# Performance work log

Measured on AMD Instinct MI355X. Metric: run time of the kernel, lower is better.

The kernel has to match this reference:

```python
import jax, jax.numpy as jnp
import numpy as np

EPS = 1e-5


def _bn_relu(h, gamma, beta):
    # BatchNorm1d in training mode: stats over all but the last (channel) dim
    m = h.reshape(-1, h.shape[-1])
    mu = jnp.mean(m, axis=0)
    var = jnp.var(m, axis=0)
    return jax.nn.relu((h - mu) * jax.lax.rsqrt(var + EPS) * gamma + beta)


def setup_inputs() -> dict:
    key = jax.random.key(0)
    ks = jax.random.split(key, 16)
    B, N, D, OUT = 64, 64, 64, 128
    T = 2 * D          # object_tuple_size = 128
    HG, HF = 256, 128  # hidden_dim_g, hidden_dim_f

    def lin(k, i, o):
        return (jax.random.normal(k, (i, o), jnp.float32) / np.sqrt(i).astype(np.float32),
                jnp.zeros((o,), jnp.float32))

    inp = {"x": jax.random.normal(ks[0], (B, N, D), jnp.float32)}
    # G: depth-3 Linear-BN-ReLU, dims T -> HG -> HG -> T
    for i, (a, b) in enumerate([(T, HG), (HG, HG), (HG, T)]):
        W, bb = lin(ks[1 + i], a, b)
        inp[f"gW{i}"] = W
        inp[f"gb{i}"] = bb
        inp[f"gg{i}"] = jnp.ones((b,), jnp.float32)
        inp[f"gB{i}"] = jnp.zeros((b,), jnp.float32)
    # F: depth-2 Linear-BN-ReLU, dims T -> HF -> T, then Linear(T, OUT)
    for i, (a, b) in enumerate([(T, HF), (HF, T)]):
        W, bb = lin(ks[5 + i], a, b)
        inp[f"fW{i}"] = W
        inp[f"fb{i}"] = bb
        inp[f"fg{i}"] = jnp.ones((b,), jnp.float32)
        inp[f"fB{i}"] = jnp.zeros((b,), jnp.float32)
    inp["foW"], inp["fob"] = lin(ks[8], T, OUT)
    return inp


def reference(x, gW0, gb0, gg0, gB0, gW1, gb1, gg1, gB1, gW2, gb2, gg2, gB2,
              fW0, fb0, fg0, fB0, fW1, fb1, fg1, fB1, foW, fob):
    B, N, D = x.shape
    # GroupObjectsIntoPairs: all ordered pairs -> (B, N*N, 2D)
    xi = jnp.broadcast_to(x[:, :, None, :], (B, N, N, D))
    xj = jnp.broadcast_to(x[:, None, :, :], (B, N, N, D))
    h = jnp.concatenate([xi, xj], axis=-1).reshape(B, N * N, 2 * D)
    # G: per-pair MLP
    for W, b, g, be in ((gW0, gb0, gg0, gB0), (gW1, gb1, gg1, gB1), (gW2, gb2, gg2, gB2)):
        h = _bn_relu(h @ W + b, g, be)
    # sum over pair dimension (no layer norm)
    s = h.sum(axis=1)  # (B, 2D)
    # F: MLP + final linear
    for W, b, g, be in ((fW0, fb0, fg0, fB0), (fW1, fb1, fg1, fB1)):
        s = _bn_relu(s @ W + b, g, be)
    return s @ foW + fob  # (B, OUT)
```

## Files before the change

kernel.cpp:

```cpp
#include <hip/hip_runtime.h>


typedef _Float16 half8 __attribute__((ext_vector_type(8)));
typedef _Float16 half4_t __attribute__((ext_vector_type(4)));
typedef float float4_t __attribute__((ext_vector_type(4)));
typedef float float2_t __attribute__((ext_vector_type(2)));
typedef unsigned int uint2_t __attribute__((ext_vector_type(2)));

static constexpr float kEps = 1e-5f;
static constexpr float kM = 262144.f;

static constexpr size_t OFF_U   = 0;
static constexpr size_t OFF_V   = OFF_U  + (size_t)4096*256*4;
static constexpr size_t OFF_UP  = OFF_V  + (size_t)4096*256*4;
static constexpr size_t OFF_VP  = OFF_UP + (size_t)4096*256*2;
static constexpr size_t OFF_W1T = OFF_VP + (size_t)4096*256*2;
static constexpr size_t OFF_W2T = OFF_W1T + (size_t)256*256*2;
static constexpr size_t OFF_Z1  = OFF_W2T + (size_t)128*256*2;
static constexpr size_t OFF_C0S = OFF_Z1 + (size_t)262144*256;
static constexpr size_t OFF_C0T = OFF_C0S + 1024;
static constexpr size_t OFF_ST0 = OFF_C0T + 1024;
static constexpr size_t OFF_ST1 = OFF_ST0 + (size_t)64*4*256*4;
static constexpr size_t OFF_ST2 = OFF_ST1 + (size_t)32*512*4;
static constexpr size_t OFF_SB  = OFF_ST2 + (size_t)32*256*4;
static constexpr size_t OFF_FST0 = OFF_SB + (size_t)64*128*4;
static constexpr size_t OFF_FST1 = OFF_FST0 + 1024;
static constexpr int ZERO_FLOATS = (64*4*256 + 32*512 + 32*256 + 64*128 + 256 + 256);
static constexpr size_t OFF_FZ0  = OFF_FST1 + 1024;
static constexpr size_t OFF_FZ1  = OFF_FZ0 + (size_t)64*128*4;
static constexpr size_t OFF_Z2   = OFF_FZ1 + (size_t)64*128*4;

static __device__ inline half8 relu8(half8 s) {
#pragma unroll
  for (int e = 0; e < 8; ++e) s[e] = s[e] > (_Float16)0 ? s[e] : (_Float16)0;
  return s;
}

static __device__ inline uint2_t pack_fp8x8(half8 hv) {
  int lo = 0, hi = 0;
  lo = __builtin_amdgcn_cvt_pk_fp8_f32((float)hv[0], (float)hv[1], lo, false);
  lo = __builtin_amdgcn_cvt_pk_fp8_f32((float)hv[2], (float)hv[3], lo, true);
  hi = __builtin_amdgcn_cvt_pk_fp8_f32((float)hv[4], (float)hv[5], hi, false);
  hi = __builtin_amdgcn_cvt_pk_fp8_f32((float)hv[6], (float)hv[7], hi, true);
  uint2_t o = {(unsigned)lo, (unsigned)hi};
  return o;
}

__global__ __launch_bounds__(256) void k_wt(const float* __restrict__ gW1,
                                            const float* __restrict__ gW2,
                                            _Float16* __restrict__ W1T,
                                            _Float16* __restrict__ W2T,
                                            float* __restrict__ zbuf) {
  int idx = blockIdx.x * 256 + threadIdx.x;
  if (idx < 65536) {
    int n = idx >> 8, k = idx & 255;
    W1T[idx] = (_Float16)gW1[k * 256 + n];
  } else if (idx < 98304) {
    int j = idx - 65536;
    int n = j >> 8, k = j & 255;
    W2T[j] = (_Float16)gW2[k * 128 + n];
  }
  if (idx < ZERO_FLOATS) zbuf[idx] = 0.f;
}

__global__ __launch_bounds__(256) void k_prep(const float* __restrict__ x,
                                              const float* __restrict__ gW0,
                                              float* __restrict__ U,
                                              float* __restrict__ V,
                                              float* __restrict__ st0) {
  __shared__ __align__(16) float sX[32 * 64];
  __shared__ __align__(16) float sZ[32 * 128];
  int t = threadIdx.x;
  int p0 = blockIdx.x * 32;
  int by = blockIdx.y;
  int hsel = by >> 1;
  int cbase = (by & 1) * 128;
#pragma unroll
  for (int it = 0; it < 2; ++it) {
    int f4 = (it * 256 + t) * 4;
    *(float4_t*)(sX + f4) = *(const float4_t*)(x + (size_t)p0 * 64 + f4);
  }
  __syncthreads();
  int r = t >> 3, cg = (t & 7) * 16;
  const float* Wb = gW0 + (size_t)(hsel * 64) * 256 + cbase + cg;
  float acc[16];
#pragma unroll
  for (int j = 0; j < 16; ++j) acc[j] = 0.f;
  for (int k = 0; k < 64; ++k) {
    float xv = sX[r * 64 + k];
    const float4_t* wr = (const float4_t*)(Wb + (size_t)k * 256);
    float4_t w0 = wr[0], w1 = wr[1], w2 = wr[2], w3 = wr[3];
#pragma unroll
    for (int j = 0; j < 4; ++j) {
      acc[j]      += xv * w0[j];
      acc[4 + j]  += xv * w1[j];
      acc[8 + j]  += xv * w2[j];
      acc[12 + j] += xv * w3[j];
    }
  }
  float* outp = (hsel ? V : U) + (size_t)(p0 + r) * 256 + cbase + cg;
#pragma unroll
  for (int q = 0; q < 4; ++q) {
    float4_t o = {acc[q * 4], acc[q * 4 + 1], acc[q * 4 + 2], acc[q * 4 + 3]};
    *(float4_t*)(outp + q * 4) = o;
  }
#pragma unroll
  for (int j = 0; j < 16; ++j) sZ[r * 128 + cg + j] = acc[j];
  __syncthreads();
  if (t < 128) {
    float S = 0.f, S2 = 0.f;
#pragma unroll
    for (int rr = 0; rr < 32; ++rr) {
      float z = sZ[rr * 128 + t];
      S += z;
      S2 += z * z;
    }
    int b = blockIdx.x >> 1;
    atomicAdd(st0 + (size_t)(b * 4 + hsel * 2 + 0) * 256 + cbase + t, S);
    atomicAdd(st0 + (size_t)(b * 4 + hsel * 2 + 1) * 256 + cbase + t, S2);
  }
}

__global__ __launch_bounds__(256) void k_bn0(const float* __restrict__ st0,
                                             const float* __restrict__ gb0,
                                             const float* __restrict__ gg0,
                                             const float* __restrict__ gB0,
                                             float* __restrict__ c0s,
                                             float* __restrict__ c0t) {
  int c = threadIdx.x;
  float su = 0, su2 = 0, sv = 0, sv2 = 0, cross = 0;
  for (int b = 0; b < 64; ++b) {
    float a  = st0[(b * 4 + 0) * 256 + c];
    float a2 = st0[(b * 4 + 1) * 256 + c];
    float v  = st0[(b * 4 + 2) * 256 + c];
    float v2 = st0[(b * 4 + 3) * 256 + c];
    su += a; su2 += a2; sv += v; sv2 += v2; cross += a * v;
  }
  float b0 = gb0[c];
  float sumz  = 64.f * (su + sv) + kM * b0;
  float sumzz = 64.f * (su2 + sv2) + 2.f * cross + 2.f * b0 * 64.f * (su + sv) + kM * b0 * b0;
  float mu = sumz / kM;
  float var = sumzz / kM - mu * mu;
  float sc = gg0[c] * rsqrtf(var + kEps);
  c0s[c] = sc;
  c0t[c] = gB0[c] + sc * (b0 - mu);
}

__global__ __launch_bounds__(256) void k_uv(const float* __restrict__ U,
                                            const float* __restrict__ V,
                                            const float* __restrict__ c0s,
                                            const float* __restrict__ c0t,
                                            _Float16* __restrict__ Up,
                                            _Float16* __restrict__ Vp) {
  int idx = blockIdx.x * 256 + threadIdx.x;
  int e4 = idx * 4;
  int c4 = e4 & 255;
  float4_t u = *(const float4_t*)(U + e4);
  float4_t v = *(const float4_t*)(V + e4);
  float4_t s = *(const float4_t*)(c0s + c4);
  float4_t tt = *(const float4_t*)(c0t + c4);
  half4_t hu, hv;
#pragma unroll
  for (int e = 0; e < 4; ++e) {
    hu[e] = (_Float16)(u[e] * s[e] + tt[e]);
    hv[e] = (_Float16)(v[e] * s[e]);
  }
  *(half4_t*)(Up + e4) = hu;
  *(half4_t*)(Vp + e4) = hv;
}

__global__ __launch_bounds__(256) void k_gemm1(const _Float16* __restrict__ Up,
                                               const _Float16* __restrict__ Vp,
                                               const _Float16* __restrict__ W1T,
                                               const float* __restrict__ gb1,
                                               unsigned char* __restrict__ Z1,
                                               float* __restrict__ stats1) {
  __shared__ __align__(16) char smem[2 * 128 * 72 * 2];
  _Float16* sA = (_Float16*)smem;
  _Float16* sW = (_Float16*)(smem + 128 * 72 * 2);
  _Float16* sO = (_Float16*)smem;

  const int t = threadIdx.x;
  const int bx = blockIdx.x;
  const int n0 = blockIdx.y * 128;
  const int b = bx >> 5;
  const int i0 = (bx & 31) * 2;
  const long R0 = (long)bx * 128;

  const int wid = t >> 6, L = t & 63;
  const int wrow = wid >> 1, wcol = wid & 1;
  const int quad = L >> 4, l15 = L & 15;

  const int prow = t >> 2;
  const int pk = (t & 3) * 16;

  const _Float16* UpI0 = Up + (size_t)(b * 64 + i0) * 256;
  const _Float16* UpI1 = UpI0 + 256;
  const _Float16* VpJ  = Vp + (size_t)(b * 64 + prow) * 256;

  float4_t acc[4][4];
#pragma unroll
  for (int mt = 0; mt < 4; ++mt)
#pragma unroll
    for (int nt = 0; nt < 4; ++nt) acc[mt][nt] = (float4_t){0.f, 0.f, 0.f, 0.f};

  for (int kc = 0; kc < 4; ++kc) {
    __syncthreads();
    {
      const int kg = kc * 64 + pk;
      half8 va = *(const half8*)(VpJ + kg);
      half8 vb = *(const half8*)(VpJ + kg + 8);
      half8 u0a = *(const half8*)(UpI0 + kg);
      half8 u0b = *(const half8*)(UpI0 + kg + 8);
      half8 u1a = *(const half8*)(UpI1 + kg);
      half8 u1b = *(const half8*)(UpI1 + kg + 8);
      *(half8*)(sA + prow * 72 + pk)            = relu8(u0a + va);
      *(half8*)(sA + prow * 72 + pk + 8)        = relu8(u0b + vb);
      *(half8*)(sA + (64 + prow) * 72 + pk)     = relu8(u1a + va);
      *(half8*)(sA + (64 + prow) * 72 + pk + 8) = relu8(u1b + vb);
    }
#pragma unroll
    for (int it = 0; it < 4; ++it) {
      int flat = it * 256 + t;
      int row = flat >> 3, c8 = (flat & 7) * 8;
      *(half8*)(sW + row * 72 + c8) =
          *(const half8*)(W1T + (size_t)(n0 + row) * 256 + kc * 64 + c8);
    }
    __syncthreads();
#pragma unroll
    for (int ks = 0; ks < 2; ++ks) {
      const int kk = ks * 32 + quad * 8;
      half8 afr[4];
#pragma unroll
      for (int mt = 0; mt < 4; ++mt)
        afr[mt] = *(const half8*)(sA + (wrow * 64 + mt * 16 + l15) * 72 + kk);
      half8 bfr[4];
#pragma unroll
      for (int nt = 0; nt < 4; ++nt)
        bfr[nt] = *(const half8*)(sW + (wcol * 64 + nt * 16 + l15) * 72 + kk);
#pragma unroll
      for (int mt = 0; mt < 4; ++mt)
#pragma unroll
        for (int nt = 0; nt < 4; ++nt)
          acc[mt][nt] = __builtin_amdgcn_mfma_f32_16x16x32_f16(afr[mt], bfr[nt],
                                                               acc[mt][nt], 0, 0, 0);
    }
  }

  __syncthreads();
  const int rep = bx & 31;
#pragma unroll
  for (int nt = 0; nt < 4; ++nt) {
    const int lcol = wcol * 64 + nt * 16 + l15;
    const float b1c = gb1[n0 + lcol];
    float sz = 0.f, szz = 0.f;
#pragma unroll
    for (int mt = 0; mt < 4; ++mt) {
      const int lrow = wrow * 64 + mt * 16 + quad * 4;
#pragma unroll
      for (int r = 0; r < 4; ++r) {
        float z = acc[mt][nt][r] + b1c;
        sO[(lrow + r) * 136 + lcol] = (_Float16)z;
        sz += z;
        szz += z * z;
      }
    }
    sz += __shfl_xor(sz, 16, 64);
    sz += __shfl_xor(sz, 32, 64);
    szz += __shfl_xor(szz, 16, 64);
    szz += __shfl_xor(szz, 32, 64);
    if (quad == 0) {
      atomicAdd(stats1 + rep * 512 + n0 + lcol, sz);
      atomicAdd(stats1 + rep * 512 + 256 + n0 + lcol, szz);
    }
  }
  __syncthreads();
#pragma unroll
  for (int it = 0; it < 8; ++it) {
    int cid = it * 256 + t;
    int row = cid >> 4, ch = (cid & 15) * 8;
    half8 hv = *(const half8*)(sO + row * 136 + ch);
    uint2_t o = pack_fp8x8(hv);
    *(uint2_t*)(Z1 + (size_t)(R0 + row) * 256 + n0 + ch) = o;
  }
}

__global__ __launch_bounds__(256) void k_gemm2(const unsigned char* __restrict__ Z1,
                                               const _Float16* __restrict__ W2T,
                                               const float* __restrict__ st1,
                                               const float* __restrict__ gg1,
                                               const float* __restrict__ gB1,
                                               const float* __restrict__ gb2,
                                               unsigned char* __restrict__ Z2,
                                               float* __restrict__ stats2) {
  __shared__ __align__(16) char smem[2 * 128 * 72 * 2];
  _Float16* sA = (_Float16*)smem;
  _Float16* sW = (_Float16*)(smem + 128 * 72 * 2);
  _Float16* sO = (_Float16*)smem;
  __shared__ __align__(16) float sS[256];
  __shared__ __align__(16) float sT[256];
  const int t = threadIdx.x;
  const int bx = blockIdx.x;
  const long R0 = (long)bx * 128;

  {
    float S = 0.f, S2 = 0.f;
#pragma unroll
    for (int rp = 0; rp < 32; ++rp) {
      S += st1[rp * 512 + t];
      S2 += st1[rp * 512 + 256 + t];
    }
    float mu = S / kM;
    float var = S2 / kM - mu * mu;
    float sc = gg1[t] * rsqrtf(var + kEps);
    sS[t] = sc;
    sT[t] = gB1[t] - sc * mu;
  }

  const int wid = t >> 6, L = t & 63;
  const int wrow = wid >> 1, wcol = wid & 1;
  const int quad = L >> 4, l15 = L & 15;

  float4_t acc[4][4];
#pragma unroll
  for (int mt = 0; mt < 4; ++mt)
#pragma unroll
    for (int nt = 0; nt < 4; ++nt) acc[mt][nt] = (float4_t){0.f, 0.f, 0.f, 0.f};

  for (int kc = 0; kc < 4; ++kc) {
    __syncthreads();
#pragma unroll
    for (int it = 0; it < 2; ++it) {
      int flat = it * 256 + t;
      int row = flat >> 3, k8 = (flat & 7) * 8;
      int kg = kc * 64 + k8;
      float4_t s0 = *(const float4_t*)(sS + kg);
      float4_t s1 = *(const float4_t*)(sS + kg + 4);
      float4_t t0 = *(const float4_t*)(sT + kg);
      float4_t t1 = *(const float4_t*)(sT + kg + 4);
#pragma unroll
      for (int h = 0; h < 2; ++h) {
        int rr = row + h * 64;
        uint2_t p = *(const uint2_t*)(Z1 + ((size_t)R0 + rr) * 256 + kg);
        float2_t f0 = __builtin_amdgcn_cvt_pk_f32_fp8((int)p[0], false);
        float2_t f1 = __builtin_amdgcn_cvt_pk_f32_fp8((int)p[0], true);
        float2_t f2 = __builtin_amdgcn_cvt_pk_f32_fp8((int)p[1], false);
        float2_t f3 = __builtin_amdgcn_cvt_pk_f32_fp8((int)p[1], true);
        half8 ov;
        ov[0] = (_Float16)fmaxf(f0[0] * s0[0] + t0[0], 0.f);
        ov[1] = (_Float16)fmaxf(f0[1] * s0[1] + t0[1], 0.f);
        ov[2] = (_Float16)fmaxf(f1[0] * s0[2] + t0[2], 0.f);
        ov[3] = (_Float16)fmaxf(f1[1] * s0[3] + t0[3], 0.f);
        ov[4] = (_Float16)fmaxf(f2[0] * s1[0] + t1[0], 0.f);
        ov[5] = (_Float16)fmaxf(f2[1] * s1[1] + t1[1], 0.f);
        ov[6] = (_Float16)fmaxf(f3[0] * s1[2] + t1[2], 0.f);
        ov[7] = (_Float16)fmaxf(f3[1] * s1[3] + t1[3], 0.f);
        *(half8*)(sA + rr * 72 + k8) = ov;
      }
    }
#pragma unroll
    for (int it = 0; it < 4; ++it) {
      int flat = it * 256 + t;
      int row = flat >> 3, k8 = (flat & 7) * 8;
      *(half8*)(sW + row * 72 + k8) =
          *(const half8*)(W2T + (size_t)row * 256 + kc * 64 + k8);
    }
    __syncthreads();
#pragma unroll
    for (int ks = 0; ks < 2; ++ks) {
      const int kk = ks * 32 + quad * 8;
      half8 afr[4];
#pragma unroll
      for (int mt = 0; mt < 4; ++mt)
        afr[mt] = *(const half8*)(sA + (wrow * 64 + mt * 16 + l15) * 72 + kk);
      half8 bfr[4];
#pragma unroll
      for (int nt = 0; nt < 4; ++nt)
        bfr[nt] = *(const half8*)(sW + (wcol * 64 + nt * 16 + l15) * 72 + kk);
#pragma unroll
      for (int mt = 0; mt < 4; ++mt)
#pragma unroll
        for (int nt = 0; nt < 4; ++nt)
          acc[mt][nt] = __builtin_amdgcn_mfma_f32_16x16x32_f16(afr[mt], bfr[nt],
                                                               acc[mt][nt], 0, 0, 0);
    }
  }

  __syncthreads();
  const int rep = bx & 31;
#pragma unroll
  for (int nt = 0; nt < 4; ++nt) {
    const int lcol = wcol * 64 + nt * 16 + l15;
    const float b2c = gb2[lcol];
    float sz = 0.f, szz = 0.f;
#pragma unroll
    for (int mt = 0; mt < 4; ++mt) {
      const int lrow = wrow * 64 + mt * 16 + quad * 4;
#pragma unroll
      for (int r = 0; r < 4; ++r) {
        float z = acc[mt][nt][r] + b2c;
        sO[(lrow + r) * 136 + lcol] = (_Float16)z;
        sz += z;
        szz += z * z;
      }
    }
    sz += __shfl_xor(sz, 16, 64);
    sz += __shfl_xor(sz, 32, 64);
    szz += __shfl_xor(szz, 16, 64);
    szz += __shfl_xor(szz, 32, 64);
    if (quad == 0) {
      atomicAdd(stats2 + rep * 256 + lcol, sz);
      atomicAdd(stats2 + rep * 256 + 128 + lcol, szz);
    }
  }
  __syncthreads();
#pragma unroll
  for (int it = 0; it < 8; ++it) {
    int cid = it * 256 + t;
    int row = cid >> 4, ch = (cid & 15) * 8;
    half8 hv = *(const half8*)(sO + row * 136 + ch);
    uint2_t o = pack_fp8x8(hv);
    *(uint2_t*)(Z2 + (size_t)(R0 + row) * 128 + ch) = o;
  }
}

__global__ __launch_bounds__(256) void k_red(const unsigned char* __restrict__ Z2,
                                             const float* __restrict__ st2,
                                             const float* __restrict__ gg2,
                                             const float* __restrict__ gB2,
                                             float* __restrict__ sbuf) {
  __shared__ float sR[256 * 8];
  __shared__ __align__(16) float sS2[128];
  __shared__ __align__(16) float sT2[128];
  const int t = threadIdx.x;
  const int bx = blockIdx.x;
  const int b = bx >> 5;
  const long row0 = (long)bx * 128;

  if (t < 128) {
    float S = 0.f, S2 = 0.f;
#pragma unroll
    for (int rp = 0; rp < 32; ++rp) {
      S += st2[rp * 256 + t];
      S2 += st2[rp * 256 + 128 + t];
    }
    float mu = S / kM;
    float var = S2 / kM - mu * mu;
    float sc = gg2[t] * rsqrtf(var + kEps);
    sS2[t] = sc;
    sT2[t] = gB2[t] - sc * mu;
  }
  __syncthreads();

  const int rr = t >> 4;
  const int c8 = (t & 15) * 8;
  float4_t s0 = *(const float4_t*)(sS2 + c8);
  float4_t s1 = *(const float4_t*)(sS2 + c8 + 4);
  float4_t t0 = *(const float4_t*)(sT2 + c8);
  float4_t t1 = *(const float4_t*)(sT2 + c8 + 4);

  float acc[8];
#pragma unroll
  for (int e = 0; e < 8; ++e) acc[e] = 0.f;
#pragma unroll
  for (int it = 0; it < 8; ++it) {
    long row = row0 + it * 16 + rr;
    uint2_t p = *(const uint2_t*)(Z2 + row * 128 + c8);
    float2_t f0 = __builtin_amdgcn_cvt_pk_f32_fp8((int)p[0], false);
    float2_t f1 = __builtin_amdgcn_cvt_pk_f32_fp8((int)p[0], true);
    float2_t f2 = __builtin_amdgcn_cvt_pk_f32_fp8((int)p[1], false);
    float2_t f3 = __builtin_amdgcn_cvt_pk_f32_fp8((int)p[1], true);
    acc[0] += fmaxf(s0[0] * f0[0] + t0[0], 0.f);
    acc[1] += fmaxf(s0[1] * f0[1] + t0[1], 0.f);
    acc[2] += fmaxf(s0[2] * f1[0] + t0[2], 0.f);
    acc[3] += fmaxf(s0[3] * f1[1] + t0[3], 0.f);
    acc[4] += fmaxf(s1[0] * f2[0] + t1[0], 0.f);
    acc[5] += fmaxf(s1[1] * f2[1] + t1[1], 0.f);
    acc[6] += fmaxf(s1[2] * f3[0] + t1[2], 0.f);
    acc[7] += fmaxf(s1[3] * f3[1] + t1[3], 0.f);
  }
#pragma unroll
  for (int e = 0; e < 8; ++e) sR[t * 8 + e] = acc[e];
  __syncthreads();
  if (t < 128) {
    float S = 0.f;
#pragma unroll
    for (int rr2 = 0; rr2 < 16; ++rr2) S += sR[rr2 * 128 + t];
    atomicAdd(sbuf + b * 128 + t, S);
  }
}

template <bool APPLY_BN, bool STATS>
__global__ __launch_bounds__(256) void k_fg(const float* __restrict__ in,
                                            const float* __restrict__ prevStats,
                                            const float* __restrict__ g,
                                            const float* __restrict__ B,
                                            const float* __restrict__ W,
                                            const float* __restrict__ bias,
                                            float* __restrict__ zout,
                                            float* __restrict__ stats) {
  __shared__ __align__(16) float sIn[8 * 128];
  __shared__ __align__(16) float sZ[8 * 128];
  __shared__ __align__(16) float sCs[128];
  __shared__ __align__(16) float sCt[128];
  const int t = threadIdx.x;
  const int r0 = blockIdx.x * 8;

  if (APPLY_BN) {
    if (t < 128) {
      float S = prevStats[t], S2 = prevStats[128 + t];
      float mu = S / 64.f;
      float var = S2 / 64.f - mu * mu;
      float sc = g[t] * rsqrtf(var + kEps);
      sCs[t] = sc;
      sCt[t] = B[t] - sc * mu;
    }
    __syncthreads();
  }
  {
    int flat = t * 4;
    int col = flat & 127;
    float4_t v = *(const float4_t*)(in + (size_t)r0 * 128 + flat);
    if (APPLY_BN) {
      float4_t s = *(const float4_t*)(sCs + col);
      float4_t sh = *(const float4_t*)(sCt + col);
#pragma unroll
      for (int e = 0; e < 4; ++e) v[e] = fmaxf(s[e] * v[e] + sh[e], 0.f);
    }
    *(float4_t*)(sIn + flat) = v;
  }
  __syncthreads();

  const int r = t >> 5;
  const int c4 = (t & 31) * 4;
  float4_t acc = *(const float4_t*)(bias + c4);
  for (int k = 0; k < 128; ++k) {
    float xv = sIn[r * 128 + k];
    float4_t w = *(const float4_t*)(W + (size_t)k * 128 + c4);
#pragma unroll
    for (int e = 0; e < 4; ++e) acc[e] += xv * w[e];
  }
  *(float4_t*)(zout + (size_t)(r0 + r) * 128 + c4) = acc;

  if (STATS) {
    *(float4_t*)(sZ + r * 128 + c4) = acc;
    __syncthreads();
    if (t < 128) {
      float S = 0.f, S2 = 0.f;
#pragma unroll
      for (int rr = 0; rr < 8; ++rr) {
        float z = sZ[rr * 128 + t];
        S += z;
        S2 += z * z;
      }
      atomicAdd(stats + t, S);
      atomicAdd(stats + 128 + t, S2);
    }
  }
}

extern "C" void kernel_launch(void* const* d_in, const int* in_sizes, int n_in,
                              void* d_out, int out_size, void* d_ws, size_t ws_size,
                              hipStream_t stream) {
  (void)in_sizes; (void)n_in; (void)out_size; (void)ws_size;
  const float* x   = (const float*)d_in[0];
  const float* gW0 = (const float*)d_in[1];
  const float* gb0 = (const float*)d_in[2];
  const float* gg0 = (const float*)d_in[3];
  const float* gB0 = (const float*)d_in[4];
  const float* gW1 = (const float*)d_in[5];
  const float* gb1 = (const float*)d_in[6];
  const float* gg1 = (const float*)d_in[7];
  const float* gB1 = (const float*)d_in[8];
  const float* gW2 = (const float*)d_in[9];
  const float* gb2 = (const float*)d_in[10];
  const float* gg2 = (const float*)d_in[11];
  const float* gB2 = (const float*)d_in[12];
  const float* fW0 = (const float*)d_in[13];
  const float* fb0 = (const float*)d_in[14];
  const float* fg0 = (const float*)d_in[15];
  const float* fB0 = (const float*)d_in[16];
  const float* fW1 = (const float*)d_in[17];
  const float* fb1 = (const float*)d_in[18];
  const float* fg1 = (const float*)d_in[19];
  const float* fB1 = (const float*)d_in[20];
  const float* foW = (const float*)d_in[21];
  const float* fob = (const float*)d_in[22];
  float* out = (float*)d_out;

  char* ws = (char*)d_ws;
  float*    U    = (float*)(ws + OFF_U);
  float*    V    = (float*)(ws + OFF_V);
  _Float16* Up   = (_Float16*)(ws + OFF_UP);
  _Float16* Vp   = (_Float16*)(ws + OFF_VP);
  _Float16* W1T  = (_Float16*)(ws + OFF_W1T);
  _Float16* W2T  = (_Float16*)(ws + OFF_W2T);
  unsigned char* Z1 = (unsigned char*)(ws + OFF_Z1);
  float*    c0s  = (float*)(ws + OFF_C0S);
  float*    c0t  = (float*)(ws + OFF_C0T);
  float*    st0  = (float*)(ws + OFF_ST0);
  float*    st1  = (float*)(ws + OFF_ST1);
  float*    st2  = (float*)(ws + OFF_ST2);
  float*    sbuf = (float*)(ws + OFF_SB);
  float*    fst0 = (float*)(ws + OFF_FST0);
  float*    fst1 = (float*)(ws + OFF_FST1);
  float*    fz0  = (float*)(ws + OFF_FZ0);
  float*    fz1  = (float*)(ws + OFF_FZ1);
  unsigned char* Z2 = (unsigned char*)(ws + OFF_Z2);

  k_wt<<<386, 256, 0, stream>>>(gW1, gW2, W1T, W2T, st0);
  k_prep<<<dim3(128, 4), 256, 0, stream>>>(x, gW0, U, V, st0);
  k_bn0<<<1, 256, 0, stream>>>(st0, gb0, gg0, gB0, c0s, c0t);
  k_uv<<<1024, 256, 0, stream>>>(U, V, c0s, c0t, Up, Vp);
  k_gemm1<<<dim3(2048, 2), 256, 0, stream>>>(Up, Vp, W1T, gb1, Z1, st1);
  k_gemm2<<<2048, 256, 0, stream>>>(Z1, W2T, st1, gg1, gB1, gb2, Z2, st2);
  k_red<<<2048, 256, 0, stream>>>(Z2, st2, gg2, gB2, sbuf);
  k_fg<false, true><<<8, 256, 0, stream>>>(sbuf, nullptr, nullptr, nullptr,
                                           fW0, fb0, fz0, fst0);
  k_fg<true, true><<<8, 256, 0, stream>>>(fz0, fst0, fg0, fB0,
                                          fW1, fb1, fz1, fst1);
  k_fg<true, false><<<8, 256, 0, stream>>>(fz1, fst1, fg1, fB1,
                                           foW, fob, out, nullptr);
}
```

Baseline: 285.4 us.

## Compute full 256-column tile per block in gemm1 with 512 threads

The first pair GEMM now has each block cover all 256 output columns with 8 waves, instead of launching two blocks per row tile that each cover 128 columns. The fused relu(U+V) A-tile is therefore built once per row tile rather than twice, halving redundant gather and elementwise work. The fp8 store is staged through shared memory in two column halves. The cost is larger LDS use per block and bigger blocks, which may lower occupancy.

Result: slower. 307.6 us (+7.8%).

```diff
diff --git a/kernel.cpp b/kernel.cpp
--- a/kernel.cpp
+++ b/kernel.cpp
@@ -169,30 +169,29 @@
   *(half4_t*)(Vp + e4) = hv;
 }
 
-__global__ __launch_bounds__(256) void k_gemm1(const _Float16* __restrict__ Up,
+__global__ __launch_bounds__(512) void k_gemm1(const _Float16* __restrict__ Up,
                                                const _Float16* __restrict__ Vp,
                                                const _Float16* __restrict__ W1T,
                                                const float* __restrict__ gb1,
                                                unsigned char* __restrict__ Z1,
                                                float* __restrict__ stats1) {
-  __shared__ __align__(16) char smem[2 * 128 * 72 * 2];
+  __shared__ __align__(16) char smem[55296];
   _Float16* sA = (_Float16*)smem;
-  _Float16* sW = (_Float16*)(smem + 128 * 72 * 2);
+  _Float16* sW = (_Float16*)(smem + 18432);
   _Float16* sO = (_Float16*)smem;
 
   const int t = threadIdx.x;
   const int bx = blockIdx.x;
-  const int n0 = blockIdx.y * 128;
   const int b = bx >> 5;
   const int i0 = (bx & 31) * 2;
   const long R0 = (long)bx * 128;
 
   const int wid = t >> 6, L = t & 63;
-  const int wrow = wid >> 1, wcol = wid & 1;
+  const int wrow = wid >> 2, wcol = wid & 3;
   const int quad = L >> 4, l15 = L & 15;
 
-  const int prow = t >> 2;
-  const int pk = (t & 3) * 16;
+  const int prow = t >> 3;
+  const int pk8 = (t & 7) * 8;
 
   const _Float16* UpI0 = Up + (size_t)(b * 64 + i0) * 256;
   const _Float16* UpI1 = UpI0 + 256;
@@ -207,24 +206,19 @@
   for (int kc = 0; kc < 4; ++kc) {
     __syncthreads();
     {
-      const int kg = kc * 64 + pk;
+      const int kg = kc * 64 + pk8;
       half8 va = *(const half8*)(VpJ + kg);
-      half8 vb = *(const half8*)(VpJ + kg + 8);
-      half8 u0a = *(const half8*)(UpI0 + kg);
-      half8 u0b = *(const half8*)(UpI0 + kg + 8);
-      half8 u1a = *(const half8*)(UpI1 + kg);
-      half8 u1b = *(const half8*)(UpI1 + kg + 8);
-      *(half8*)(sA + prow * 72 + pk)            = relu8(u0a + va);
-      *(half8*)(sA + prow * 72 + pk + 8)        = relu8(u0b + vb);
-      *(half8*)(sA + (64 + prow) * 72 + pk)     = relu8(u1a + va);
-      *(half8*)(sA + (64 + prow) * 72 + pk + 8) = relu8(u1b + vb);
+      half8 u0 = *(const half8*)(UpI0 + kg);
+      half8 u1 = *(const half8*)(UpI1 + kg);
+      *(half8*)(sA + prow * 72 + pk8)        = relu8(u0 + va);
+      *(half8*)(sA + (64 + prow) * 72 + pk8) = relu8(u1 + va);
     }
 #pragma unroll
     for (int it = 0; it < 4; ++it) {
-      int flat = it * 256 + t;
+      int flat = it * 512 + t;
       int row = flat >> 3, c8 = (flat & 7) * 8;
       *(half8*)(sW + row * 72 + c8) =
-          *(const half8*)(W1T + (size_t)(n0 + row) * 256 + kc * 64 + c8);
+          *(const half8*)(W1T + (size_t)row * 256 + kc * 64 + c8);
     }
     __syncthreads();
 #pragma unroll
@@ -247,41 +241,57 @@
     }
   }
 
-  __syncthreads();
   const int rep = bx & 31;
 #pragma unroll
   for (int nt = 0; nt < 4; ++nt) {
-    const int lcol = wcol * 64 + nt * 16 + l15;
-    const float b1c = gb1[n0 + lcol];
+    const int col = wcol * 64 + nt * 16 + l15;
+    const float b1c = gb1[col];
     float sz = 0.f, szz = 0.f;
 #pragma unroll
-    for (int mt = 0; mt < 4; ++mt) {
-      const int lrow = wrow * 64 + mt * 16 + quad * 4;
+    for (int mt = 0; mt < 4; ++mt)
 #pragma unroll
       for (int r = 0; r < 4; ++r) {
         float z = acc[mt][nt][r] + b1c;
-        sO[(lrow + r) * 136 + lcol] = (_Float16)z;
+        acc[mt][nt][r] = z;
         sz += z;
         szz += z * z;
       }
-    }
     sz += __shfl_xor(sz, 16, 64);
     sz += __shfl_xor(sz, 32, 64);
     szz += __shfl_xor(szz, 16, 64);
     szz += __shfl_xor(szz, 32, 64);
     if (quad == 0) {
-      atomicAdd(stats1 + rep * 512 + n0 + lcol, sz);
-      atomicAdd(stats1 + rep * 512 + 256 + n0 + lcol, szz);
-    }
-  }
-  __syncthreads();
-#pragma unroll
-  for (int it = 0; it < 8; ++it) {
-    int cid = it * 256 + t;
-    int row = cid >> 4, ch = (cid & 15) * 8;
-    half8 hv = *(const half8*)(sO + row * 136 + ch);
-    uint2_t o = pack_fp8x8(hv);
-    *(uint2_t*)(Z1 + (size_t)(R0 + row) * 256 + n0 + ch) = o;
+      atomicAdd(stats1 + rep * 512 + col, sz);
+      atomicAdd(stats1 + rep * 512 + 256 + col, szz);
+    }
+  }
+
+#pragma unroll
+  for (int p = 0; p < 2; ++p) {
+    __syncthreads();
+    if ((wcol >> 1) == p) {
+      const int colh = (wcol & 1) * 64;
+#pragma unroll
+      for (int nt = 0; nt < 4; ++nt) {
+        const int lc = colh + nt * 16 + l15;
+#pragma unroll
+        for (int mt = 0; mt < 4; ++mt) {
+          const int lrow = wrow * 64 + mt * 16 + quad * 4;
+#pragma unroll
+          for (int r = 0; r < 4; ++r)
+            sO[(lrow + r) * 136 + lc] = (_Float16)acc[mt][nt][r];
+        }
+      }
+    }
+    __syncthreads();
+#pragma unroll
+    for (int it = 0; it < 4; ++it) {
+      int cid = it * 512 + t;
+      int row = cid >> 4, ch = (cid & 15) * 8;
+      half8 hv = *(const half8*)(sO + row * 136 + ch);
+      uint2_t o = pack_fp8x8(hv);
+      *(uint2_t*)(Z1 + (size_t)(R0 + row) * 256 + p * 128 + ch) = o;
+    }
   }
 }
 
@@ -612,7 +622,7 @@
   k_prep<<<dim3(128, 4), 256, 0, stream>>>(x, gW0, U, V, st0);
   k_bn0<<<1, 256, 0, stream>>>(st0, gb0, gg0, gB0, c0s, c0t);
   k_uv<<<1024, 256, 0, stream>>>(U, V, c0s, c0t, Up, Vp);
-  k_gemm1<<<dim3(2048, 2), 256, 0, stream>>>(Up, Vp, W1T, gb1, Z1, st1);
+  k_gemm1<<<2048, 512, 0, stream>>>(Up, Vp, W1T, gb1, Z1, st1);
   k_gemm2<<<2048, 256, 0, stream>>>(Z1, W2T, st1, gg1, gB1, gb2, Z2, st2);
   k_red<<<2048, 256, 0, stream>>>(Z2, st2, gg2, gB2, sbuf);
   k_fg<false, true><<<8, 256, 0, stream>>>(sbuf, nullptr, nullptr, nullptr,
```

## Retile gemm1 to 64x256 tiles covering full N per block

Applied to the files above, without the earlier changes.

The first pair-GEMM changes from 128-row by 128-column tiles on a 2D grid to 64-row by 256-column tiles on a 1D grid of 4096 blocks. Each block handles one object i against all j and covers every output channel. This removes the recomputation of the A tile (relu(U+V)) across the two column halves and makes Z1 row writes contiguous. In exchange, each block loads the whole W1T slice per k-chunk, needs more shared memory (46 KB), and gets less A reuse per MFMA.

New measurement: 302.8 us. 1.06x slower.

```diff
diff --git a/kernel.cpp b/kernel.cpp
--- a/kernel.cpp
+++ b/kernel.cpp
@@ -175,28 +175,25 @@
                                                const float* __restrict__ gb1,
                                                unsigned char* __restrict__ Z1,
                                                float* __restrict__ stats1) {
-  __shared__ __align__(16) char smem[2 * 128 * 72 * 2];
+  __shared__ __align__(16) char smem[46080];
   _Float16* sA = (_Float16*)smem;
-  _Float16* sW = (_Float16*)(smem + 128 * 72 * 2);
+  _Float16* sW = (_Float16*)(smem + 9216);
   _Float16* sO = (_Float16*)smem;
 
   const int t = threadIdx.x;
   const int bx = blockIdx.x;
-  const int n0 = blockIdx.y * 128;
-  const int b = bx >> 5;
-  const int i0 = (bx & 31) * 2;
-  const long R0 = (long)bx * 128;
+  const int b = bx >> 6;
+  const int i = bx & 63;
+  const long R0 = (long)bx * 64;
 
   const int wid = t >> 6, L = t & 63;
-  const int wrow = wid >> 1, wcol = wid & 1;
   const int quad = L >> 4, l15 = L & 15;
 
   const int prow = t >> 2;
   const int pk = (t & 3) * 16;
 
-  const _Float16* UpI0 = Up + (size_t)(b * 64 + i0) * 256;
-  const _Float16* UpI1 = UpI0 + 256;
-  const _Float16* VpJ  = Vp + (size_t)(b * 64 + prow) * 256;
+  const _Float16* UpI = Up + (size_t)(b * 64 + i) * 256;
+  const _Float16* VpJ = Vp + (size_t)(b * 64 + prow) * 256;
 
   float4_t acc[4][4];
 #pragma unroll
@@ -208,23 +205,19 @@
     __syncthreads();
     {
       const int kg = kc * 64 + pk;
+      half8 ua = *(const half8*)(UpI + kg);
+      half8 ub = *(const half8*)(UpI + kg + 8);
       half8 va = *(const half8*)(VpJ + kg);
       half8 vb = *(const half8*)(VpJ + kg + 8);
-      half8 u0a = *(const half8*)(UpI0 + kg);
-      half8 u0b = *(const half8*)(UpI0 + kg + 8);
-      half8 u1a = *(const half8*)(UpI1 + kg);
-      half8 u1b = *(const half8*)(UpI1 + kg + 8);
-      *(half8*)(sA + prow * 72 + pk)            = relu8(u0a + va);
-      *(half8*)(sA + prow * 72 + pk + 8)        = relu8(u0b + vb);
-      *(half8*)(sA + (64 + prow) * 72 + pk)     = relu8(u1a + va);
-      *(half8*)(sA + (64 + prow) * 72 + pk + 8) = relu8(u1b + vb);
-    }
-#pragma unroll
-    for (int it = 0; it < 4; ++it) {
+      *(half8*)(sA + prow * 72 + pk)     = relu8(ua + va);
+      *(half8*)(sA + prow * 72 + pk + 8) = relu8(ub + vb);
+    }
+#pragma unroll
+    for (int it = 0; it < 8; ++it) {
       int flat = it * 256 + t;
       int row = flat >> 3, c8 = (flat & 7) * 8;
       *(half8*)(sW + row * 72 + c8) =
-          *(const half8*)(W1T + (size_t)(n0 + row) * 256 + kc * 64 + c8);
+          *(const half8*)(W1T + (size_t)row * 256 + kc * 64 + c8);
     }
     __syncthreads();
 #pragma unroll
@@ -233,11 +226,11 @@
       half8 afr[4];
 #pragma unroll
       for (int mt = 0; mt < 4; ++mt)
-        afr[mt] = *(const half8*)(sA + (wrow * 64 + mt * 16 + l15) * 72 + kk);
+        afr[mt] = *(const half8*)(sA + (mt * 16 + l15) * 72 + kk);
       half8 bfr[4];
 #pragma unroll
       for (int nt = 0; nt < 4; ++nt)
-        bfr[nt] = *(const half8*)(sW + (wcol * 64 + nt * 16 + l15) * 72 + kk);
+        bfr[nt] = *(const half8*)(sW + (wid * 64 + nt * 16 + l15) * 72 + kk);
 #pragma unroll
       for (int mt = 0; mt < 4; ++mt)
 #pragma unroll
@@ -248,40 +241,51 @@
   }
 
   __syncthreads();
+
   const int rep = bx & 31;
 #pragma unroll
   for (int nt = 0; nt < 4; ++nt) {
-    const int lcol = wcol * 64 + nt * 16 + l15;
-    const float b1c = gb1[n0 + lcol];
+    const int col = wid * 64 + nt * 16 + l15;
+    const float b1c = gb1[col];
     float sz = 0.f, szz = 0.f;
 #pragma unroll
-    for (int mt = 0; mt < 4; ++mt) {
-      const int lrow = wrow * 64 + mt * 16 + quad * 4;
+    for (int mt = 0; mt < 4; ++mt)
 #pragma unroll
       for (int r = 0; r < 4; ++r) {
         float z = acc[mt][nt][r] + b1c;
-        sO[(lrow + r) * 136 + lcol] = (_Float16)z;
+        acc[mt][nt][r] = z;
         sz += z;
         szz += z * z;
       }
-    }
     sz += __shfl_xor(sz, 16, 64);
     sz += __shfl_xor(sz, 32, 64);
     szz += __shfl_xor(szz, 16, 64);
     szz += __shfl_xor(szz, 32, 64);
     if (quad == 0) {
-      atomicAdd(stats1 + rep * 512 + n0 + lcol, sz);
-      atomicAdd(stats1 + rep * 512 + 256 + n0 + lcol, szz);
+      atomicAdd(stats1 + rep * 512 + col, sz);
+      atomicAdd(stats1 + rep * 512 + 256 + col, szz);
+    }
+  }
+
+#pragma unroll
+  for (int nt = 0; nt < 4; ++nt) {
+    const int col = wid * 64 + nt * 16 + l15;
+#pragma unroll
+    for (int mt = 0; mt < 4; ++mt) {
+      const int lrow = mt * 16 + quad * 4;
+#pragma unroll
+      for (int r = 0; r < 4; ++r)
+        sO[(lrow + r) * 264 + col] = (_Float16)acc[mt][nt][r];
     }
   }
   __syncthreads();
 #pragma unroll
   for (int it = 0; it < 8; ++it) {
     int cid = it * 256 + t;
-    int row = cid >> 4, ch = (cid & 15) * 8;
-    half8 hv = *(const half8*)(sO + row * 136 + ch);
+    int row = cid >> 5, ch = (cid & 31) * 8;
+    half8 hv = *(const half8*)(sO + row * 264 + ch);
     uint2_t o = pack_fp8x8(hv);
-    *(uint2_t*)(Z1 + (size_t)(R0 + row) * 256 + n0 + ch) = o;
+    *(uint2_t*)(Z1 + (size_t)(R0 + row) * 256 + ch) = o;
   }
 }
 
@@ -612,7 +616,7 @@
   k_prep<<<dim3(128, 4), 256, 0, stream>>>(x, gW0, U, V, st0);
   k_bn0<<<1, 256, 0, stream>>>(st0, gb0, gg0, gB0, c0s, c0t);
   k_uv<<<1024, 256, 0, stream>>>(U, V, c0s, c0t, Up, Vp);
-  k_gemm1<<<dim3(2048, 2), 256, 0, stream>>>(Up, Vp, W1T, gb1, Z1, st1);
+  k_gemm1<<<4096, 256, 0, stream>>>(Up, Vp, W1T, gb1, Z1, st1);
   k_gemm2<<<2048, 256, 0, stream>>>(Z1, W2T, st1, gg1, gB1, gb2, Z2, st2);
   k_red<<<2048, 256, 0, stream>>>(Z2, st2, gg2, gB2, sbuf);
   k_fg<false, true><<<8, 256, 0, stream>>>(sbuf, nullptr, nullptr, nullptr,
```
